# Kernel tuning notes

Measured on AMD Instinct MI355X. Metric: run time of the kernel, lower is better.

Reference implementation:

```python
import jax, jax.numpy as jnp
import numpy as np

PRE_NMS_TOP_N = 1024
POST_NMS_TOP_N = 256
NMS_THRESH = 0.7
MIN_SIZE = 4.0
SCORE_THRESH = 0.1
BASE_SIZE = 1024.0
SCALE = 0.25            # feature stride = 1/SCALE = 4
IMG_H, IMG_W = 1024.0, 1024.0
NEG_INF = -1e30
CAP = 8                 # max vertices of 4-gon intersect 4-gon


def setup_inputs() -> dict:
    key = jax.random.key(0)
    k1, k2 = jax.random.split(key)
    N, A, H, W = 2, 1, 256, 256
    objectness = jax.random.normal(k1, (N, A, H, W), dtype=jnp.float32)
    box_regression = jax.random.uniform(k2, (N, A * 5, H, W), dtype=jnp.float32) * 0.05
    return {"objectness": objectness, "box_regression": box_regression}


def eastbox2rbox(reg, H, W):
    # reg: (H*W, 5) -> rotated boxes (H*W, 5) in xywha (angle in degrees)
    jy, jx = jnp.meshgrid(jnp.arange(H, dtype=reg.dtype), jnp.arange(W, dtype=reg.dtype), indexing="ij")
    cx0 = (jx / SCALE).reshape(-1)
    cy0 = (jy / SCALE).reshape(-1)
    t = reg[:, 0] * BASE_SIZE
    r = reg[:, 1] * BASE_SIZE
    b = reg[:, 2] * BASE_SIZE
    l = reg[:, 3] * BASE_SIZE
    ang = (reg[:, 4] - 0.5) * 90.0
    w = l + r
    h = t + b
    xc = cx0 + 0.5 * (r - l)
    yc = cy0 + 0.5 * (b - t)
    return jnp.stack([xc, yc, w, h, ang], axis=-1)


def rbox_corners(box):
    # box: (5,) xywha -> (4,2) CCW corners
    th = box[4] * (jnp.pi / 180.0)
    c, s = jnp.cos(th), jnp.sin(th)
    dx = jnp.array([-0.5, 0.5, 0.5, -0.5], box.dtype) * box[2]
    dy = jnp.array([-0.5, -0.5, 0.5, 0.5], box.dtype) * box[3]
    return jnp.stack([box[0] + dx * c - dy * s, box[1] + dx * s + dy * c], axis=-1)


def clip_halfplane(poly, n, p1, p2):
    # Sutherland-Hodgman clip of a convex polygon (CAP,2) with n valid verts
    # against the half-plane left of directed edge p1->p2.
    M = poly.shape[0]
    idx = jnp.arange(M)
    valid = idx < n
    nxt = poly[jnp.where(idx + 1 < n, idx + 1, 0)]
    e = p2 - p1
    d_cur = e[0] * (poly[:, 1] - p1[1]) - e[1] * (poly[:, 0] - p1[0])
    d_nxt = e[0] * (nxt[:, 1] - p1[1]) - e[1] * (nxt[:, 0] - p1[0])
    in_cur = d_cur >= 0.0
    in_nxt = d_nxt >= 0.0
    denom = d_cur - d_nxt
    safe = jnp.where(jnp.abs(denom) > 1e-9, denom, 1.0)
    t = d_cur / safe
    inter = poly + t[:, None] * (nxt - poly)
    emit_cur = in_cur & valid
    emit_int = (in_cur != in_nxt) & valid
    pts = jnp.stack([poly, inter], axis=1).reshape(2 * M, 2)
    flags = jnp.stack([emit_cur, emit_int], axis=1).reshape(2 * M)
    pos = jnp.where(flags, jnp.cumsum(flags) - 1, M)  # M = dropped
    out = jnp.zeros((M, 2), poly.dtype).at[pos].set(jnp.where(flags[:, None], pts, 0.0), mode="drop")
    return out, jnp.sum(flags)


def intersect_area(pa, pb):
    # area of convex intersection of two 4-gons (each (4,2), CCW)
    poly = jnp.zeros((CAP, 2), pa.dtype).at[:4].set(pa)
    n = jnp.asarray(4, jnp.int32)
    for k in range(4):
        poly, n = clip_halfplane(poly, n, pb[k], pb[(k + 1) % 4])
    idx = jnp.arange(CAP)
    valid = idx < n
    nxt = poly[jnp.where(idx + 1 < n, idx + 1, 0)]
    cr = poly[:, 0] * nxt[:, 1] - nxt[:, 0] * poly[:, 1]
    area = 0.5 * jnp.abs(jnp.sum(jnp.where(valid, cr, 0.0)))
    return jnp.where(n >= 3, area, 0.0)


def riou(a, b):
    inter = intersect_area(rbox_corners(a), rbox_corners(b))
    union = a[2] * a[3] + b[2] * b[3] - inter
    return inter / jnp.maximum(union, 1e-9)


def greedy_nms(iou_mat, valid, thresh):
    K = valid.shape[0]
    ar = jnp.arange(K)

    def body(i, state):
        keep, sup = state
        is_keep = valid[i] & jnp.logical_not(sup[i])
        keep = keep.at[i].set(is_keep)
        sup = sup | (is_keep & (iou_mat[i] > thresh) & (ar > i))
        return keep, sup

    keep, _ = jax.lax.fori_loop(0, K, body, (jnp.zeros(K, bool), jnp.zeros(K, bool)))
    return keep


def process_image(obj, reg):
    A, H, W = obj.shape
    scores = obj.transpose(1, 2, 0).reshape(-1)       # (H*W*A,)
    reg5 = reg[:5].transpose(1, 2, 0).reshape(-1, 5)  # (H*W, 5)
    rboxes = eastbox2rbox(reg5, H, W)
    top_scores, top_idx = jax.lax.top_k(scores, PRE_NMS_TOP_N)
    boxes = rboxes[top_idx]
    valid = top_scores > SCORE_THRESH                 # eval-mode score thresh (masked, not dropped)
    # clip_to_image: clamp rotated-box centers into the image
    boxes = boxes.at[:, 0].set(jnp.clip(boxes[:, 0], 0.0, IMG_W - 1.0))
    boxes = boxes.at[:, 1].set(jnp.clip(boxes[:, 1], 0.0, IMG_H - 1.0))
    # remove_small_boxes
    valid = valid & (boxes[:, 2] >= MIN_SIZE) & (boxes[:, 3] >= MIN_SIZE)
    # full rotated IoU matrix, row-by-row to bound memory
    iou_mat = jax.lax.map(lambda a: jax.vmap(lambda b: riou(a, b))(boxes), boxes)
    keep = greedy_nms(iou_mat, valid, NMS_THRESH)
    sel = jnp.where(keep, top_scores, NEG_INF)
    fin_scores, fin_idx = jax.lax.top_k(sel, POST_NMS_TOP_N)
    fin_boxes = boxes[fin_idx]
    fin_valid = keep[fin_idx]
    out = jnp.concatenate([fin_boxes, fin_scores[:, None]], axis=-1)  # (post, 6) = xywha + score
    return jnp.where(fin_valid[:, None], out, 0.0)


def reference(objectness, box_regression):
    return jax.vmap(process_image)(objectness, box_regression)
```

## Files before the change

kernel.cpp:

```cpp
#include <hip/hip_runtime.h>
#include <hip/hip_bf16.h>

#define N_IMG 2
#define HW 65536
#define PRE 1024
#define POST 256
#define NBIN 4096
#define SORTN 4096
#define NMS_THR 0.7f
#define SCORE_T 0.1f
#define MIN_SZ 4.0f

__device__ __forceinline__ unsigned int fkey(float f) {
    unsigned int u = __float_as_uint(f);
    return u ^ ((u & 0x80000000u) ? 0xFFFFFFFFu : 0x80000000u);
}
__device__ __forceinline__ float unfkey(unsigned int k) {
    unsigned int u = (k & 0x80000000u) ? (k ^ 0x80000000u) : ~k;
    return __uint_as_float(u);
}
__device__ __forceinline__ unsigned long long readlane64(unsigned long long v, int l) {
    unsigned int lo = (unsigned int)__builtin_amdgcn_readlane((int)(unsigned int)v, l);
    unsigned int hi = (unsigned int)__builtin_amdgcn_readlane((int)(unsigned int)(v >> 32), l);
    return ((unsigned long long)hi << 32) | (unsigned long long)lo;
}

__global__ __launch_bounds__(1024) void k_front(const float* __restrict__ obj,
                                                unsigned int* phist,
                                                unsigned long long* masks,
                                                unsigned int* cnts) {
    __shared__ unsigned int lh[NBIN];
    int img = blockIdx.x >> 3;
    int seg = blockIdx.x & 7;
    for (int i = threadIdx.x; i < NBIN; i += 1024) lh[i] = 0u;
    {
        unsigned long long* mz = masks + (size_t)blockIdx.x * 2048;
        mz[threadIdx.x] = 0ULL;
        mz[threadIdx.x + 1024] = 0ULL;
    }
    if (blockIdx.x == 0 && threadIdx.x < 8) cnts[threadIdx.x] = 0u;
    __syncthreads();
    const float4* o4 = (const float4*)(obj + (size_t)img * HW);
    int base = seg * 2048;
#pragma unroll
    for (int k = 0; k < 2; ++k) {
        float4 v = o4[base + threadIdx.x + k * 1024];
        atomicAdd(&lh[fkey(v.x) >> 20], 1u);
        atomicAdd(&lh[fkey(v.y) >> 20], 1u);
        atomicAdd(&lh[fkey(v.z) >> 20], 1u);
        atomicAdd(&lh[fkey(v.w) >> 20], 1u);
    }
    __syncthreads();
    unsigned int* ph = phist + (size_t)blockIdx.x * NBIN;
    for (int i = threadIdx.x; i < NBIN; i += 1024) ph[i] = lh[i];
}

__global__ void k_findbin(const unsigned int* __restrict__ phist, unsigned int* selB) {
    __shared__ unsigned int lh[NBIN];
    __shared__ unsigned int chunk[256];
    int img = blockIdx.x;
    int t = threadIdx.x;
    for (int c = 0; c < 16; ++c) {
        int b = c * 256 + t;
        unsigned int v = 0;
#pragma unroll
        for (int q = 0; q < 8; ++q) v += phist[(size_t)(img * 8 + q) * NBIN + b];
        lh[b] = v;
    }
    __syncthreads();
    unsigned int s = 0;
    for (int k = 0; k < 16; ++k) s += lh[t * 16 + k];
    chunk[t] = s;
    __syncthreads();
    if (t == 0) {
        unsigned int run = 0;
        int c;
        for (c = 255; c >= 0; --c) {
            if (run + chunk[c] >= PRE) break;
            run += chunk[c];
        }
        unsigned int B = 0;
        for (int b = c * 16 + 15; b >= c * 16; --b) {
            if (run + lh[b] >= PRE) { B = (unsigned int)b; break; }
            run += lh[b];
        }
        selB[img] = B;
    }
}

__global__ __launch_bounds__(256) void k_compact(const float* __restrict__ obj,
                                                 const unsigned int* __restrict__ selB,
                                                 unsigned int* cnts, unsigned long long* cbuf) {
    __shared__ unsigned long long lbuf[1024];
    __shared__ unsigned int lcnt, lbase;
    int t = blockIdx.x * 256 + threadIdx.x;
    const float4* o4 = (const float4*)obj;
#pragma unroll
    for (int k = 0; k < 2; ++k) {
        if (threadIdx.x == 0) lcnt = 0;
        __syncthreads();
        int p = t + k * 16384;
        int img = p >> 14;
        unsigned int B = selB[img];
        float4 v = o4[p];
        float vs[4] = {v.x, v.y, v.z, v.w};
#pragma unroll
        for (int c = 0; c < 4; ++c) {
            unsigned int key = fkey(vs[c]);
            if ((key >> 20) >= B) {
                unsigned int i = (unsigned int)((p & 16383) * 4 + c);
                unsigned int pos = atomicAdd(&lcnt, 1u);
                lbuf[pos] = ((unsigned long long)key << 32) |
                            (unsigned long long)(0xFFFFFFFFu - i);
            }
        }
        __syncthreads();
        if (threadIdx.x == 0) lbase = atomicAdd(&cnts[img], lcnt);
        __syncthreads();
        unsigned int n = lcnt, base = lbase;
        for (unsigned int q = threadIdx.x; q < n; q += 256) {
            unsigned int gp = base + q;
            if (gp < SORTN) cbuf[img * SORTN + gp] = lbuf[q];
        }
        __syncthreads();
    }
}

__global__ __launch_bounds__(256) void k_rankdec(const unsigned int* __restrict__ cnts,
                                                 const unsigned long long* __restrict__ cbuf,
                                                 const float* __restrict__ boxreg,
                                                 float* boxes, float* corn, float4* circ,
                                                 unsigned int* varr, float* tscr) {
    __shared__ unsigned long long keys[SORTN];
    int img = blockIdx.x >> 4;
    int slice = blockIdx.x & 15;
    unsigned int M = cnts[img]; if (M > SORTN) M = SORTN;
    for (unsigned int i = threadIdx.x; i < M; i += 256) keys[i] = cbuf[img * SORTN + i];
    __syncthreads();
    unsigned int cid = (unsigned int)slice * 256 + threadIdx.x;
    if (cid >= M) return;
    unsigned long long cv = keys[cid];
    unsigned int r = 0;
    for (unsigned int j = 0; j < M; ++j) r += (keys[j] > cv) ? 1u : 0u;
    if (r >= PRE) return;

    int g = img * PRE + (int)r;
    unsigned int key = (unsigned int)(cv >> 32);
    unsigned int idx = (0xFFFFFFFFu - (unsigned int)(cv & 0xFFFFFFFFULL)) & 0xFFFFu;
    float sc = unfkey(key);
    int h = (int)(idx >> 8);
    int w = (int)(idx & 255u);
    const float* rg = boxreg + (size_t)img * 5 * HW;
    float t_ = rg[0 * HW + idx] * 1024.0f;
    float rr = rg[1 * HW + idx] * 1024.0f;
    float bb = rg[2 * HW + idx] * 1024.0f;
    float ll = rg[3 * HW + idx] * 1024.0f;
    float ang = (rg[4 * HW + idx] - 0.5f) * 90.0f;
    float wd = ll + rr;
    float ht = t_ + bb;
    float xc = (float)w * 4.0f + 0.5f * (rr - ll);
    float yc = (float)h * 4.0f + 0.5f * (bb - t_);
    xc = fminf(fmaxf(xc, 0.0f), 1023.0f);
    yc = fminf(fmaxf(yc, 0.0f), 1023.0f);
    bool valid = (sc > SCORE_T) && (wd >= MIN_SZ) && (ht >= MIN_SZ);

    float* bx = boxes + (size_t)g * 5;
    bx[0] = xc; bx[1] = yc; bx[2] = wd; bx[3] = ht; bx[4] = ang;
    tscr[g] = sc;
    varr[g] = valid ? 1u : 0u;

    float th = ang * (float)(3.14159265358979323846 / 180.0);
    float c = cosf(th), s = sinf(th);
    const float dxs[4] = {-0.5f, 0.5f, 0.5f, -0.5f};
    const float dys[4] = {-0.5f, -0.5f, 0.5f, 0.5f};
    float* cr = corn + (size_t)g * 8;
#pragma unroll
    for (int k = 0; k < 4; ++k) {
        float dx = dxs[k] * wd, dy = dys[k] * ht;
        cr[2 * k]     = xc + dx * c - dy * s;
        cr[2 * k + 1] = yc + dx * s + dy * c;
    }
    circ[g] = make_float4(xc, yc, 0.5f * sqrtf(wd * wd + ht * ht) + 0.01f, wd * ht);
}

__global__ __launch_bounds__(256) void k_pairclip(const float4* __restrict__ circ,
                                                  const float* __restrict__ corn,
                                                  unsigned long long* masks) {
    __shared__ float SPX[8][256], SPY[8][256], SQX[8][256], SQY[8][256];
    __shared__ unsigned int plist[1280];
    __shared__ unsigned int pcnt;
    int tid = threadIdx.x;
    if (tid == 0) pcnt = 0;
    __syncthreads();
    int t0 = blockIdx.x * 256 + tid;
    for (int k = 0; k < 16; ++k) {
        int p = t0 + k * 131072;
        int img = p >> 20;
        int r = p & 1048575;
        int i = r >> 10, j = r & 1023;
        if (j > i) {
            float4 a = circ[img * PRE + i];
            float4 b = circ[img * PRE + j];
            float dx = b.x - a.x, dy = b.y - a.y, rr = a.z + b.z;
            if (dx * dx + dy * dy <= rr * rr)
                plist[atomicAdd(&pcnt, 1u)] =
                    ((unsigned int)img << 20) | ((unsigned int)i << 10) | (unsigned int)j;
        }
        __syncthreads();
        unsigned int n = pcnt;
        if (n >= 1024 || k == 15) {
            for (unsigned int q = tid; q < n; q += 256) {
                unsigned int pr = plist[q];
                int im = (int)(pr >> 20);
                int bi = (int)((pr >> 10) & 1023);
                int bj = (int)(pr & 1023);
                int ra = im * PRE + bi, rb = im * PRE + bj;
                const float4* ca = (const float4*)(corn + (size_t)ra * 8);
                float4 a0 = ca[0], a1 = ca[1];
                const float4* cb = (const float4*)(corn + (size_t)rb * 8);
                float4 b0 = cb[0], b1 = cb[1];
                float cbx[4] = {b0.x, b0.z, b1.x, b1.z};
                float cby[4] = {b0.y, b0.w, b1.y, b1.w};
                SPX[0][tid] = a0.x; SPY[0][tid] = a0.y;
                SPX[1][tid] = a0.z; SPY[1][tid] = a0.w;
                SPX[2][tid] = a1.x; SPY[2][tid] = a1.y;
                SPX[3][tid] = a1.z; SPY[3][tid] = a1.w;
                int n2 = 4;
#pragma unroll
                for (int e = 0; e < 4; ++e) {
                    float (*PX)[256] = (e & 1) ? SQX : SPX;
                    float (*PY)[256] = (e & 1) ? SQY : SPY;
                    float (*QX)[256] = (e & 1) ? SPX : SQX;
                    float (*QY)[256] = (e & 1) ? SPY : SQY;
                    float p1x = cbx[e], p1y = cby[e];
                    int e2 = (e + 1) & 3;
                    float ex = cbx[e2] - p1x, ey = cby[e2] - p1y;
                    int m = 0;
                    for (int kk = 0; kk < n2; ++kk) {
                        int kn = (kk + 1 < n2) ? kk + 1 : 0;
                        float cx_ = PX[kk][tid], cy_ = PY[kk][tid];
                        float nx_ = PX[kn][tid], ny_ = PY[kn][tid];
                        float dc = ex * (cy_ - p1y) - ey * (cx_ - p1x);
                        float dn = ex * (ny_ - p1y) - ey * (nx_ - p1x);
                        bool ic = dc >= 0.0f;
                        bool inx = dn >= 0.0f;
                        if (ic && m < 8) { QX[m][tid] = cx_; QY[m][tid] = cy_; ++m; }
                        if ((ic != inx) && m < 8) {
                            float den = dc - dn;
                            float safe = (fabsf(den) > 1e-9f) ? den : 1.0f;
                            float tt = dc / safe;
                            QX[m][tid] = cx_ + tt * (nx_ - cx_);
                            QY[m][tid] = cy_ + tt * (ny_ - cy_);
                            ++m;
                        }
                    }
                    n2 = m;
                }
                float inter = 0.0f;
                if (n2 >= 3) {
                    float s = 0.0f;
                    for (int kk = 0; kk < n2; ++kk) {
                        int kn = (kk + 1 < n2) ? kk + 1 : 0;
                        s += SPX[kk][tid] * SPY[kn][tid] - SPX[kn][tid] * SPY[kk][tid];
                    }
                    inter = 0.5f * fabsf(s);
                }
                float uni = circ[ra].w + circ[rb].w - inter;
                float iou = inter / fmaxf(uni, 1e-9f);
                if (iou > NMS_THR)
                    atomicOr(&masks[(size_t)ra * 16 + (bj >> 6)], 1ULL << (bj & 63));
            }
            __syncthreads();
            if (tid == 0) pcnt = 0;
            __syncthreads();
        }
    }
}

__global__ __launch_bounds__(1024) void k_nms_out(const unsigned long long* __restrict__ masks,
                                                  const unsigned int* __restrict__ varr,
                                                  const float* __restrict__ boxes,
                                                  const float* __restrict__ tscr,
                                                  float* __restrict__ out) {
    __shared__ unsigned long long lm[PRE * 16];
    __shared__ unsigned long long vmw_s[16];
    __shared__ unsigned short keptIdx[POST];
    __shared__ int sTotal;
    int img = blockIdx.x;
    int t = threadIdx.x;
    const unsigned long long* mbase = masks + (size_t)img * PRE * 16;
    {
        const ulonglong2* src = (const ulonglong2*)mbase;
        ulonglong2* dst = (ulonglong2*)lm;
#pragma unroll
        for (int k = 0; k < 8; ++k) dst[t + k * 1024] = src[t + k * 1024];
    }
    {
        unsigned long long bal = __ballot(varr[img * PRE + t] != 0u);
        if ((t & 63) == 0) vmw_s[t >> 6] = bal;
    }
    __syncthreads();

    if (t < 64) {
        int lane = t;
        int lw = lane & 15;
        unsigned long long vmw = vmw_s[lw];
        unsigned long long supw = 0ULL;
        int cnt = 0;
        for (int b = 0; b < 16 && cnt < POST; ++b) {
            unsigned long long avail = readlane64(vmw, b) & ~readlane64(supw, b);
            while (avail && cnt < POST) {
                unsigned long long a = avail;
                int d0 = __ffsll((long long)a) - 1; a &= a - 1;
                int d1 = a ? __ffsll((long long)a) - 1 : 64; a &= a - 1;
                int d2 = a ? __ffsll((long long)a) - 1 : 64; a &= a - 1;
                int d3 = a ? __ffsll((long long)a) - 1 : 64; a &= a - 1;
                int r0 = b * 64 + d0;
                int r1 = b * 64 + (d1 & 63);
                int r2 = b * 64 + (d2 & 63);
                int r3 = b * 64 + (d3 & 63);
                unsigned long long w0 = lm[r0 * 16 + lw];
                unsigned long long w1 = lm[r1 * 16 + lw];
                unsigned long long w2 = lm[r2 * 16 + lw];
                unsigned long long w3 = lm[r3 * 16 + lw];
                unsigned long long sb = readlane64(w0, b);
                supw |= w0;
                if (lane == 0) keptIdx[cnt] = (unsigned short)r0;
                ++cnt;
                if (d1 < 64 && cnt < POST && !((sb >> d1) & 1ULL)) {
                    sb |= readlane64(w1, b); supw |= w1;
                    if (lane == 0) keptIdx[cnt] = (unsigned short)r1;
                    ++cnt;
                }
                if (d2 < 64 && cnt < POST && !((sb >> d2) & 1ULL)) {
                    sb |= readlane64(w2, b); supw |= w2;
                    if (lane == 0) keptIdx[cnt] = (unsigned short)r2;
                    ++cnt;
                }
                if (d3 < 64 && cnt < POST && !((sb >> d3) & 1ULL)) {
                    sb |= readlane64(w3, b); supw |= w3;
                    if (lane == 0) keptIdx[cnt] = (unsigned short)r3;
                    ++cnt;
                }
                avail = a & ~sb;
            }
        }
        if (lane == 0) sTotal = cnt;
    }
    __syncthreads();

    int total = sTotal;
    if (t < POST) {
        float v0 = 0.f, v1 = 0.f, v2 = 0.f, v3 = 0.f, v4 = 0.f, v5 = 0.f;
        if (t < total) {
            int i = keptIdx[t];
            const float* b = boxes + (size_t)(img * PRE + i) * 5;
            v0 = b[0]; v1 = b[1]; v2 = b[2]; v3 = b[3]; v4 = b[4];
            v5 = tscr[img * PRE + i];
        }
        float* o2 = out + (size_t)(img * POST + t) * 6;
        o2[0] = v0; o2[1] = v1; o2[2] = v2; o2[3] = v3; o2[4] = v4; o2[5] = v5;
    }
}

enum : size_t {
    OFF_BOX   = 0,
    OFF_CORN  = 40960,
    OFF_CIRC  = 106496,
    OFF_VARR  = 139264,
    OFF_TSCR  = 147456,
    OFF_MASK  = 155648,
    OFF_PHIST = 417792,
    OFF_CNTS  = 679936,
    OFF_SELB  = 679968,
    OFF_CBUF  = 679984,
};

extern "C" void kernel_launch(void* const* d_in, const int* in_sizes, int n_in,
                              void* d_out, int out_size, void* d_ws, size_t ws_size,
                              hipStream_t stream) {
    const float* obj = (const float*)d_in[0];
    const float* boxreg = (const float*)d_in[1];
    float* out = (float*)d_out;

    char* w = (char*)d_ws;
    float* boxes = (float*)(w + OFF_BOX);
    float* corn = (float*)(w + OFF_CORN);
    float4* circ = (float4*)(w + OFF_CIRC);
    unsigned int* varr = (unsigned int*)(w + OFF_VARR);
    float* tscr = (float*)(w + OFF_TSCR);
    unsigned long long* masks = (unsigned long long*)(w + OFF_MASK);
    unsigned int* phist = (unsigned int*)(w + OFF_PHIST);
    unsigned int* cnts = (unsigned int*)(w + OFF_CNTS);
    unsigned int* selB = (unsigned int*)(w + OFF_SELB);
    unsigned long long* cbuf = (unsigned long long*)(w + OFF_CBUF);

    k_front<<<16, 1024, 0, stream>>>(obj, phist, masks, cnts);
    k_findbin<<<N_IMG, 256, 0, stream>>>(phist, selB);
    k_compact<<<64, 256, 0, stream>>>(obj, selB, cnts, cbuf);
    k_rankdec<<<32, 256, 0, stream>>>(cnts, cbuf, boxreg, boxes, corn, circ, varr, tscr);
    k_pairclip<<<512, 256, 0, stream>>>(circ, corn, masks);
    k_nms_out<<<N_IMG, 1024, 0, stream>>>(masks, varr, boxes, tscr, out);
}
```

Before: 88.77 us.

## Fuse the six pipeline kernels into one cooperative persistent kernel with grid syncs

Merges histogram, bin selection, compaction, rank/decode, pair clipping and NMS into a single cooperative launch of 256 blocks that separates stages with grid.sync, and keeps the multi-kernel path as a fallback if the cooperative launch fails. The aim is to remove per-kernel launch gaps and tail latency between the six small dependent kernels. In exchange, the pair-clip stage runs on 256 blocks instead of 512, so each block handles twice the pairs. The shared-memory union also grows to the largest stage (128KB for the NMS mask copy), which can limit residency or cause the cooperative launch to fail.

```diff
diff --git a/kernel.cpp b/kernel.cpp
--- a/kernel.cpp
+++ b/kernel.cpp
@@ -1,5 +1,8 @@
 #include <hip/hip_runtime.h>
 #include <hip/hip_bf16.h>
+#include <hip/hip_cooperative_groups.h>
+
+namespace cg = cooperative_groups;
 
 #define N_IMG 2
 #define HW 65536
@@ -10,6 +13,7 @@
 #define NMS_THR 0.7f
 #define SCORE_T 0.1f
 #define MIN_SZ 4.0f
+#define GRID 256
 
 __device__ __forceinline__ unsigned int fkey(float f) {
     unsigned int u = __float_as_uint(f);
@@ -25,126 +29,28 @@
     return ((unsigned long long)hi << 32) | (unsigned long long)lo;
 }
 
-__global__ __launch_bounds__(1024) void k_front(const float* __restrict__ obj,
-                                                unsigned int* phist,
-                                                unsigned long long* masks,
-                                                unsigned int* cnts) {
-    __shared__ unsigned int lh[NBIN];
-    int img = blockIdx.x >> 3;
-    int seg = blockIdx.x & 7;
-    for (int i = threadIdx.x; i < NBIN; i += 1024) lh[i] = 0u;
-    {
-        unsigned long long* mz = masks + (size_t)blockIdx.x * 2048;
-        mz[threadIdx.x] = 0ULL;
-        mz[threadIdx.x + 1024] = 0ULL;
-    }
-    if (blockIdx.x == 0 && threadIdx.x < 8) cnts[threadIdx.x] = 0u;
-    __syncthreads();
-    const float4* o4 = (const float4*)(obj + (size_t)img * HW);
-    int base = seg * 2048;
-#pragma unroll
-    for (int k = 0; k < 2; ++k) {
-        float4 v = o4[base + threadIdx.x + k * 1024];
-        atomicAdd(&lh[fkey(v.x) >> 20], 1u);
-        atomicAdd(&lh[fkey(v.y) >> 20], 1u);
-        atomicAdd(&lh[fkey(v.z) >> 20], 1u);
-        atomicAdd(&lh[fkey(v.w) >> 20], 1u);
-    }
-    __syncthreads();
-    unsigned int* ph = phist + (size_t)blockIdx.x * NBIN;
-    for (int i = threadIdx.x; i < NBIN; i += 1024) ph[i] = lh[i];
-}
-
-__global__ void k_findbin(const unsigned int* __restrict__ phist, unsigned int* selB) {
-    __shared__ unsigned int lh[NBIN];
-    __shared__ unsigned int chunk[256];
-    int img = blockIdx.x;
-    int t = threadIdx.x;
-    for (int c = 0; c < 16; ++c) {
-        int b = c * 256 + t;
-        unsigned int v = 0;
-#pragma unroll
-        for (int q = 0; q < 8; ++q) v += phist[(size_t)(img * 8 + q) * NBIN + b];
-        lh[b] = v;
-    }
-    __syncthreads();
-    unsigned int s = 0;
-    for (int k = 0; k < 16; ++k) s += lh[t * 16 + k];
-    chunk[t] = s;
-    __syncthreads();
-    if (t == 0) {
-        unsigned int run = 0;
-        int c;
-        for (c = 255; c >= 0; --c) {
-            if (run + chunk[c] >= PRE) break;
-            run += chunk[c];
-        }
-        unsigned int B = 0;
-        for (int b = c * 16 + 15; b >= c * 16; --b) {
-            if (run + lh[b] >= PRE) { B = (unsigned int)b; break; }
-            run += lh[b];
-        }
-        selB[img] = B;
-    }
-}
-
-__global__ __launch_bounds__(256) void k_compact(const float* __restrict__ obj,
-                                                 const unsigned int* __restrict__ selB,
-                                                 unsigned int* cnts, unsigned long long* cbuf) {
-    __shared__ unsigned long long lbuf[1024];
-    __shared__ unsigned int lcnt, lbase;
-    int t = blockIdx.x * 256 + threadIdx.x;
-    const float4* o4 = (const float4*)obj;
-#pragma unroll
-    for (int k = 0; k < 2; ++k) {
-        if (threadIdx.x == 0) lcnt = 0;
-        __syncthreads();
-        int p = t + k * 16384;
-        int img = p >> 14;
-        unsigned int B = selB[img];
-        float4 v = o4[p];
-        float vs[4] = {v.x, v.y, v.z, v.w};
-#pragma unroll
-        for (int c = 0; c < 4; ++c) {
-            unsigned int key = fkey(vs[c]);
-            if ((key >> 20) >= B) {
-                unsigned int i = (unsigned int)((p & 16383) * 4 + c);
-                unsigned int pos = atomicAdd(&lcnt, 1u);
-                lbuf[pos] = ((unsigned long long)key << 32) |
-                            (unsigned long long)(0xFFFFFFFFu - i);
-            }
-        }
-        __syncthreads();
-        if (threadIdx.x == 0) lbase = atomicAdd(&cnts[img], lcnt);
-        __syncthreads();
-        unsigned int n = lcnt, base = lbase;
-        for (unsigned int q = threadIdx.x; q < n; q += 256) {
-            unsigned int gp = base + q;
-            if (gp < SORTN) cbuf[img * SORTN + gp] = lbuf[q];
-        }
-        __syncthreads();
-    }
-}
-
-__global__ __launch_bounds__(256) void k_rankdec(const unsigned int* __restrict__ cnts,
-                                                 const unsigned long long* __restrict__ cbuf,
-                                                 const float* __restrict__ boxreg,
-                                                 float* boxes, float* corn, float4* circ,
-                                                 unsigned int* varr, float* tscr) {
-    __shared__ unsigned long long keys[SORTN];
-    int img = blockIdx.x >> 4;
-    int slice = blockIdx.x & 15;
-    unsigned int M = cnts[img]; if (M > SORTN) M = SORTN;
-    for (unsigned int i = threadIdx.x; i < M; i += 256) keys[i] = cbuf[img * SORTN + i];
-    __syncthreads();
-    unsigned int cid = (unsigned int)slice * 256 + threadIdx.x;
-    if (cid >= M) return;
-    unsigned long long cv = keys[cid];
-    unsigned int r = 0;
-    for (unsigned int j = 0; j < M; ++j) r += (keys[j] > cv) ? 1u : 0u;
-    if (r >= PRE) return;
-
-    int g = img * PRE + (int)r;
+struct SMemU {
+    union {
+        unsigned int hist[NBIN];
+        unsigned long long lbuf[1024];
+        unsigned long long keys[SORTN];
+        struct {
+            float SPX[8][256], SPY[8][256], SQX[8][256], SQY[8][256];
+            unsigned int plist[1280];
+        } e;
+        unsigned long long lm[PRE * 16];
+    } u;
+    unsigned int pcnt, lcnt, lbase;
+    unsigned long long vmw_s[16];
+    unsigned short keptIdx[POST];
+    int sTotal;
+};
+
+__device__ __forceinline__ void decode_one(unsigned long long cv, int img,
+                                           const float* __restrict__ boxreg,
+                                           float* boxes, float* corn, float4* circ,
+                                           unsigned int* varr, float* tscr, int r) {
+    int g = img * PRE + r;
     unsigned int key = (unsigned int)(cv >> 32);
     unsigned int idx = (0xFFFFFFFFu - (unsigned int)(cv & 0xFFFFFFFFULL)) & 0xFFFFu;
     float sc = unfkey(key);
@@ -183,11 +89,436 @@
     circ[g] = make_float4(xc, yc, 0.5f * sqrtf(wd * wd + ht * ht) + 0.01f, wd * ht);
 }
 
+template <typename E>
+__device__ __forceinline__ void clip_pair(unsigned int pr, int tid, E* e,
+                                          const float* __restrict__ corn,
+                                          const float4* __restrict__ circ,
+                                          unsigned long long* masks) {
+    int im = (int)(pr >> 20);
+    int bi = (int)((pr >> 10) & 1023);
+    int bj = (int)(pr & 1023);
+    int ra = im * PRE + bi, rb = im * PRE + bj;
+    const float4* ca = (const float4*)(corn + (size_t)ra * 8);
+    float4 a0 = ca[0], a1 = ca[1];
+    const float4* cb = (const float4*)(corn + (size_t)rb * 8);
+    float4 b0 = cb[0], b1 = cb[1];
+    float cbx[4] = {b0.x, b0.z, b1.x, b1.z};
+    float cby[4] = {b0.y, b0.w, b1.y, b1.w};
+    e->SPX[0][tid] = a0.x; e->SPY[0][tid] = a0.y;
+    e->SPX[1][tid] = a0.z; e->SPY[1][tid] = a0.w;
+    e->SPX[2][tid] = a1.x; e->SPY[2][tid] = a1.y;
+    e->SPX[3][tid] = a1.z; e->SPY[3][tid] = a1.w;
+    int n2 = 4;
+#pragma unroll
+    for (int ed = 0; ed < 4; ++ed) {
+        float (*PX)[256] = (ed & 1) ? e->SQX : e->SPX;
+        float (*PY)[256] = (ed & 1) ? e->SQY : e->SPY;
+        float (*QX)[256] = (ed & 1) ? e->SPX : e->SQX;
+        float (*QY)[256] = (ed & 1) ? e->SPY : e->SQY;
+        float p1x = cbx[ed], p1y = cby[ed];
+        int e2 = (ed + 1) & 3;
+        float ex = cbx[e2] - p1x, ey = cby[e2] - p1y;
+        int m = 0;
+        for (int kk = 0; kk < n2; ++kk) {
+            int kn = (kk + 1 < n2) ? kk + 1 : 0;
+            float cx_ = PX[kk][tid], cy_ = PY[kk][tid];
+            float nx_ = PX[kn][tid], ny_ = PY[kn][tid];
+            float dc = ex * (cy_ - p1y) - ey * (cx_ - p1x);
+            float dn = ex * (ny_ - p1y) - ey * (nx_ - p1x);
+            bool ic = dc >= 0.0f;
+            bool inx = dn >= 0.0f;
+            if (ic && m < 8) { QX[m][tid] = cx_; QY[m][tid] = cy_; ++m; }
+            if ((ic != inx) && m < 8) {
+                float den = dc - dn;
+                float safe = (fabsf(den) > 1e-9f) ? den : 1.0f;
+                float tt = dc / safe;
+                QX[m][tid] = cx_ + tt * (nx_ - cx_);
+                QY[m][tid] = cy_ + tt * (ny_ - cy_);
+                ++m;
+            }
+        }
+        n2 = m;
+    }
+    float inter = 0.0f;
+    if (n2 >= 3) {
+        float s = 0.0f;
+        for (int kk = 0; kk < n2; ++kk) {
+            int kn = (kk + 1 < n2) ? kk + 1 : 0;
+            s += e->SPX[kk][tid] * e->SPY[kn][tid] - e->SPX[kn][tid] * e->SPY[kk][tid];
+        }
+        inter = 0.5f * fabsf(s);
+    }
+    float uni = circ[ra].w + circ[rb].w - inter;
+    float iou = inter / fmaxf(uni, 1e-9f);
+    if (iou > NMS_THR)
+        atomicOr(&masks[(size_t)ra * 16 + (bj >> 6)], 1ULL << (bj & 63));
+}
+
+__global__ __launch_bounds__(256) void k_mega(const float* __restrict__ obj,
+                                              const float* __restrict__ boxreg,
+                                              float* __restrict__ out,
+                                              float* boxes, float* corn, float4* circ,
+                                              unsigned int* varr, float* tscr,
+                                              unsigned long long* masks, unsigned int* phist,
+                                              unsigned int* cnts, unsigned int* selB,
+                                              unsigned long long* cbuf) {
+    cg::grid_group grid = cg::this_grid();
+    __shared__ SMemU sm;
+    int bid = blockIdx.x;
+    int tid = threadIdx.x;
+
+    {
+        unsigned long long* mz = masks + (size_t)bid * 128;
+        if (tid < 128) mz[tid] = 0ULL;
+        if (bid == 0 && tid < 8) cnts[tid] = 0u;
+        if (bid < 16) {
+            unsigned int* lh = sm.u.hist;
+            for (int i = tid; i < NBIN; i += 256) lh[i] = 0u;
+            __syncthreads();
+            int img = bid >> 3, seg = bid & 7;
+            const float4* o4 = (const float4*)(obj + (size_t)img * HW);
+            int base = seg * 2048;
+#pragma unroll
+            for (int k = 0; k < 8; ++k) {
+                float4 v = o4[base + tid + k * 256];
+                atomicAdd(&lh[fkey(v.x) >> 20], 1u);
+                atomicAdd(&lh[fkey(v.y) >> 20], 1u);
+                atomicAdd(&lh[fkey(v.z) >> 20], 1u);
+                atomicAdd(&lh[fkey(v.w) >> 20], 1u);
+            }
+            __syncthreads();
+            unsigned int* ph = phist + (size_t)bid * NBIN;
+            for (int i = tid; i < NBIN; i += 256) ph[i] = lh[i];
+        }
+    }
+    __threadfence();
+    grid.sync();
+
+    if (bid < N_IMG) {
+        int img = bid;
+        unsigned int* lh = sm.u.hist;
+        __shared__ unsigned int chunk[256];
+        for (int c = 0; c < 16; ++c) {
+            int b = c * 256 + tid;
+            unsigned int v = 0;
+#pragma unroll
+            for (int q = 0; q < 8; ++q) v += phist[(size_t)(img * 8 + q) * NBIN + b];
+            lh[b] = v;
+        }
+        __syncthreads();
+        unsigned int s = 0;
+        for (int k = 0; k < 16; ++k) s += lh[tid * 16 + k];
+        chunk[tid] = s;
+        __syncthreads();
+        if (tid == 0) {
+            unsigned int run = 0;
+            int c;
+            for (c = 255; c >= 0; --c) {
+                if (run + chunk[c] >= PRE) break;
+                run += chunk[c];
+            }
+            unsigned int B = 0;
+            for (int b = c * 16 + 15; b >= c * 16; --b) {
+                if (run + lh[b] >= PRE) { B = (unsigned int)b; break; }
+                run += lh[b];
+            }
+            selB[img] = B;
+        }
+    }
+    __threadfence();
+    grid.sync();
+
+    if (bid < 64) {
+        int t = bid * 256 + tid;
+        const float4* o4 = (const float4*)obj;
+#pragma unroll
+        for (int k = 0; k < 2; ++k) {
+            if (tid == 0) sm.lcnt = 0;
+            __syncthreads();
+            int p = t + k * 16384;
+            int img = p >> 14;
+            unsigned int B = selB[img];
+            float4 v = o4[p];
+            float vs[4] = {v.x, v.y, v.z, v.w};
+#pragma unroll
+            for (int c = 0; c < 4; ++c) {
+                unsigned int key = fkey(vs[c]);
+                if ((key >> 20) >= B) {
+                    unsigned int i = (unsigned int)((p & 16383) * 4 + c);
+                    unsigned int pos = atomicAdd(&sm.lcnt, 1u);
+                    sm.u.lbuf[pos] = ((unsigned long long)key << 32) |
+                                     (unsigned long long)(0xFFFFFFFFu - i);
+                }
+            }
+            __syncthreads();
+            if (tid == 0) sm.lbase = atomicAdd(&cnts[img], sm.lcnt);
+            __syncthreads();
+            unsigned int n = sm.lcnt, base = sm.lbase;
+            for (unsigned int q = tid; q < n; q += 256) {
+                unsigned int gp = base + q;
+                if (gp < SORTN) cbuf[img * SORTN + gp] = sm.u.lbuf[q];
+            }
+            __syncthreads();
+        }
+    }
+    __threadfence();
+    grid.sync();
+
+    if (bid < 32) {
+        int img = bid >> 4;
+        int slice = bid & 15;
+        unsigned int M = cnts[img]; if (M > SORTN) M = SORTN;
+        for (unsigned int i = tid; i < M; i += 256) sm.u.keys[i] = cbuf[img * SORTN + i];
+        __syncthreads();
+        unsigned int cid = (unsigned int)slice * 256 + tid;
+        if (cid < M) {
+            unsigned long long cv = sm.u.keys[cid];
+            unsigned int r = 0;
+            for (unsigned int j = 0; j < M; ++j) r += (sm.u.keys[j] > cv) ? 1u : 0u;
+            if (r < PRE)
+                decode_one(cv, img, boxreg, boxes, corn, circ, varr, tscr, (int)r);
+        }
+    }
+    __threadfence();
+    grid.sync();
+
+    {
+        if (tid == 0) sm.pcnt = 0;
+        __syncthreads();
+        int t0 = bid * 256 + tid;
+        for (int k = 0; k < 32; ++k) {
+            int p = t0 + k * 65536;
+            int img = p >> 20;
+            int r = p & 1048575;
+            int i = r >> 10, j = r & 1023;
+            if (j > i) {
+                float4 a = circ[img * PRE + i];
+                float4 b = circ[img * PRE + j];
+                float dx = b.x - a.x, dy = b.y - a.y, rr = a.z + b.z;
+                if (dx * dx + dy * dy <= rr * rr)
+                    sm.u.e.plist[atomicAdd(&sm.pcnt, 1u)] =
+                        ((unsigned int)img << 20) | ((unsigned int)i << 10) | (unsigned int)j;
+            }
+            __syncthreads();
+            unsigned int n = sm.pcnt;
+            if (n >= 1024 || k == 31) {
+                for (unsigned int q = tid; q < n; q += 256)
+                    clip_pair(sm.u.e.plist[q], tid, &sm.u.e, corn, circ, masks);
+                __syncthreads();
+                if (tid == 0) sm.pcnt = 0;
+                __syncthreads();
+            }
+        }
+    }
+    __threadfence();
+    grid.sync();
+
+    if (bid < N_IMG) {
+        int img = bid;
+        {
+            const ulonglong2* src = (const ulonglong2*)(masks + (size_t)img * PRE * 16);
+            ulonglong2* dst = (ulonglong2*)sm.u.lm;
+#pragma unroll
+            for (int k = 0; k < 32; ++k) dst[tid + k * 256] = src[tid + k * 256];
+        }
+        {
+            int wv = tid >> 6, lane = tid & 63;
+#pragma unroll
+            for (int q = 0; q < 4; ++q) {
+                unsigned long long bal = __ballot(varr[img * PRE + q * 256 + tid] != 0u);
+                if (lane == 0) sm.vmw_s[q * 4 + wv] = bal;
+            }
+        }
+        __syncthreads();
+        if (tid < 64) {
+            int lane = tid;
+            int lw = lane & 15;
+            unsigned long long vmw = sm.vmw_s[lw];
+            unsigned long long supw = 0ULL;
+            int cnt = 0;
+            for (int b = 0; b < 16 && cnt < POST; ++b) {
+                unsigned long long avail = readlane64(vmw, b) & ~readlane64(supw, b);
+                while (avail && cnt < POST) {
+                    unsigned long long a = avail;
+                    int d0 = __ffsll((long long)a) - 1; a &= a - 1;
+                    int d1 = a ? __ffsll((long long)a) - 1 : 64; a &= a - 1;
+                    int d2 = a ? __ffsll((long long)a) - 1 : 64; a &= a - 1;
+                    int d3 = a ? __ffsll((long long)a) - 1 : 64; a &= a - 1;
+                    int r0 = b * 64 + d0;
+                    int r1 = b * 64 + (d1 & 63);
+                    int r2 = b * 64 + (d2 & 63);
+                    int r3 = b * 64 + (d3 & 63);
+                    unsigned long long w0 = sm.u.lm[r0 * 16 + lw];
+                    unsigned long long w1 = sm.u.lm[r1 * 16 + lw];
+                    unsigned long long w2 = sm.u.lm[r2 * 16 + lw];
+                    unsigned long long w3 = sm.u.lm[r3 * 16 + lw];
+                    unsigned long long sb = readlane64(w0, b);
+                    supw |= w0;
+                    if (lane == 0) sm.keptIdx[cnt] = (unsigned short)r0;
+                    ++cnt;
+                    if (d1 < 64 && cnt < POST && !((sb >> d1) & 1ULL)) {
+                        sb |= readlane64(w1, b); supw |= w1;
+                        if (lane == 0) sm.keptIdx[cnt] = (unsigned short)r1;
+                        ++cnt;
+                    }
+                    if (d2 < 64 && cnt < POST && !((sb >> d2) & 1ULL)) {
+                        sb |= readlane64(w2, b); supw |= w2;
+                        if (lane == 0) sm.keptIdx[cnt] = (unsigned short)r2;
+                        ++cnt;
+                    }
+                    if (d3 < 64 && cnt < POST && !((sb >> d3) & 1ULL)) {
+                        sb |= readlane64(w3, b); supw |= w3;
+                        if (lane == 0) sm.keptIdx[cnt] = (unsigned short)r3;
+                        ++cnt;
+                    }
+                    avail = a & ~sb;
+                }
+            }
+            if (lane == 0) sm.sTotal = cnt;
+        }
+        __syncthreads();
+        int total = sm.sTotal;
+        {
+            float v0 = 0.f, v1 = 0.f, v2 = 0.f, v3 = 0.f, v4 = 0.f, v5 = 0.f;
+            if (tid < total) {
+                int i = sm.keptIdx[tid];
+                const float* b = boxes + (size_t)(img * PRE + i) * 5;
+                v0 = b[0]; v1 = b[1]; v2 = b[2]; v3 = b[3]; v4 = b[4];
+                v5 = tscr[img * PRE + i];
+            }
+            float* o2 = out + (size_t)(img * POST + tid) * 6;
+            o2[0] = v0; o2[1] = v1; o2[2] = v2; o2[3] = v3; o2[4] = v4; o2[5] = v5;
+        }
+    }
+}
+
+__global__ __launch_bounds__(1024) void k_front(const float* __restrict__ obj,
+                                                unsigned int* phist,
+                                                unsigned long long* masks,
+                                                unsigned int* cnts) {
+    __shared__ unsigned int lh[NBIN];
+    int img = blockIdx.x >> 3;
+    int seg = blockIdx.x & 7;
+    for (int i = threadIdx.x; i < NBIN; i += 1024) lh[i] = 0u;
+    {
+        unsigned long long* mz = masks + (size_t)blockIdx.x * 2048;
+        mz[threadIdx.x] = 0ULL;
+        mz[threadIdx.x + 1024] = 0ULL;
+    }
+    if (blockIdx.x == 0 && threadIdx.x < 8) cnts[threadIdx.x] = 0u;
+    __syncthreads();
+    const float4* o4 = (const float4*)(obj + (size_t)img * HW);
+    int base = seg * 2048;
+#pragma unroll
+    for (int k = 0; k < 2; ++k) {
+        float4 v = o4[base + threadIdx.x + k * 1024];
+        atomicAdd(&lh[fkey(v.x) >> 20], 1u);
+        atomicAdd(&lh[fkey(v.y) >> 20], 1u);
+        atomicAdd(&lh[fkey(v.z) >> 20], 1u);
+        atomicAdd(&lh[fkey(v.w) >> 20], 1u);
+    }
+    __syncthreads();
+    unsigned int* ph = phist + (size_t)blockIdx.x * NBIN;
+    for (int i = threadIdx.x; i < NBIN; i += 1024) ph[i] = lh[i];
+}
+
+__global__ void k_findbin(const unsigned int* __restrict__ phist, unsigned int* selB) {
+    __shared__ unsigned int lh[NBIN];
+    __shared__ unsigned int chunk[256];
+    int img = blockIdx.x;
+    int t = threadIdx.x;
+    for (int c = 0; c < 16; ++c) {
+        int b = c * 256 + t;
+        unsigned int v = 0;
+#pragma unroll
+        for (int q = 0; q < 8; ++q) v += phist[(size_t)(img * 8 + q) * NBIN + b];
+        lh[b] = v;
+    }
+    __syncthreads();
+    unsigned int s = 0;
+    for (int k = 0; k < 16; ++k) s += lh[t * 16 + k];
+    chunk[t] = s;
+    __syncthreads();
+    if (t == 0) {
+        unsigned int run = 0;
+        int c;
+        for (c = 255; c >= 0; --c) {
+            if (run + chunk[c] >= PRE) break;
+            run += chunk[c];
+        }
+        unsigned int B = 0;
+        for (int b = c * 16 + 15; b >= c * 16; --b) {
+            if (run + lh[b] >= PRE) { B = (unsigned int)b; break; }
+            run += lh[b];
+        }
+        selB[img] = B;
+    }
+}
+
+__global__ __launch_bounds__(256) void k_compact(const float* __restrict__ obj,
+                                                 const unsigned int* __restrict__ selB,
+                                                 unsigned int* cnts, unsigned long long* cbuf) {
+    __shared__ unsigned long long lbuf[1024];
+    __shared__ unsigned int lcnt, lbase;
+    int t = blockIdx.x * 256 + threadIdx.x;
+    const float4* o4 = (const float4*)obj;
+#pragma unroll
+    for (int k = 0; k < 2; ++k) {
+        if (threadIdx.x == 0) lcnt = 0;
+        __syncthreads();
+        int p = t + k * 16384;
+        int img = p >> 14;
+        unsigned int B = selB[img];
+        float4 v = o4[p];
+        float vs[4] = {v.x, v.y, v.z, v.w};
+#pragma unroll
+        for (int c = 0; c < 4; ++c) {
+            unsigned int key = fkey(vs[c]);
+            if ((key >> 20) >= B) {
+                unsigned int i = (unsigned int)((p & 16383) * 4 + c);
+                unsigned int pos = atomicAdd(&lcnt, 1u);
+                lbuf[pos] = ((unsigned long long)key << 32) |
+                            (unsigned long long)(0xFFFFFFFFu - i);
+            }
+        }
+        __syncthreads();
+        if (threadIdx.x == 0) lbase = atomicAdd(&cnts[img], lcnt);
+        __syncthreads();
+        unsigned int n = lcnt, base = lbase;
+        for (unsigned int q = threadIdx.x; q < n; q += 256) {
+            unsigned int gp = base + q;
+            if (gp < SORTN) cbuf[img * SORTN + gp] = lbuf[q];
+        }
+        __syncthreads();
+    }
+}
+
+__global__ __launch_bounds__(256) void k_rankdec(const unsigned int* __restrict__ cnts,
+                                                 const unsigned long long* __restrict__ cbuf,
+                                                 const float* __restrict__ boxreg,
+                                                 float* boxes, float* corn, float4* circ,
+                                                 unsigned int* varr, float* tscr) {
+    __shared__ unsigned long long keys[SORTN];
+    int img = blockIdx.x >> 4;
+    int slice = blockIdx.x & 15;
+    unsigned int M = cnts[img]; if (M > SORTN) M = SORTN;
+    for (unsigned int i = threadIdx.x; i < M; i += 256) keys[i] = cbuf[img * SORTN + i];
+    __syncthreads();
+    unsigned int cid = (unsigned int)slice * 256 + threadIdx.x;
+    if (cid >= M) return;
+    unsigned long long cv = keys[cid];
+    unsigned int r = 0;
+    for (unsigned int j = 0; j < M; ++j) r += (keys[j] > cv) ? 1u : 0u;
+    if (r < PRE) decode_one(cv, img, boxreg, boxes, corn, circ, varr, tscr, (int)r);
+}
+
 __global__ __launch_bounds__(256) void k_pairclip(const float4* __restrict__ circ,
                                                   const float* __restrict__ corn,
                                                   unsigned long long* masks) {
-    __shared__ float SPX[8][256], SPY[8][256], SQX[8][256], SQY[8][256];
-    __shared__ unsigned int plist[1280];
+    __shared__ struct {
+        float SPX[8][256], SPY[8][256], SQX[8][256], SQY[8][256];
+        unsigned int plist[1280];
+    } e;
     __shared__ unsigned int pcnt;
     int tid = threadIdx.x;
     if (tid == 0) pcnt = 0;
@@ -203,73 +534,14 @@
             float4 b = circ[img * PRE + j];
             float dx = b.x - a.x, dy = b.y - a.y, rr = a.z + b.z;
             if (dx * dx + dy * dy <= rr * rr)
-                plist[atomicAdd(&pcnt, 1u)] =
+                e.plist[atomicAdd(&pcnt, 1u)] =
                     ((unsigned int)img << 20) | ((unsigned int)i << 10) | (unsigned int)j;
         }
         __syncthreads();
         unsigned int n = pcnt;
         if (n >= 1024 || k == 15) {
-            for (unsigned int q = tid; q < n; q += 256) {
-                unsigned int pr = plist[q];
-                int im = (int)(pr >> 20);
-                int bi = (int)((pr >> 10) & 1023);
-                int bj = (int)(pr & 1023);
-                int ra = im * PRE + bi, rb = im * PRE + bj;
-                const float4* ca = (const float4*)(corn + (size_t)ra * 8);
-                float4 a0 = ca[0], a1 = ca[1];
-                const float4* cb = (const float4*)(corn + (size_t)rb * 8);
-                float4 b0 = cb[0], b1 = cb[1];
-                float cbx[4] = {b0.x, b0.z, b1.x, b1.z};
-                float cby[4] = {b0.y, b0.w, b1.y, b1.w};
-                SPX[0][tid] = a0.x; SPY[0][tid] = a0.y;
-                SPX[1][tid] = a0.z; SPY[1][tid] = a0.w;
-                SPX[2][tid] = a1.x; SPY[2][tid] = a1.y;
-                SPX[3][tid] = a1.z; SPY[3][tid] = a1.w;
-                int n2 = 4;
-#pragma unroll
-                for (int e = 0; e < 4; ++e) {
-                    float (*PX)[256] = (e & 1) ? SQX : SPX;
-                    float (*PY)[256] = (e & 1) ? SQY : SPY;
-                    float (*QX)[256] = (e & 1) ? SPX : SQX;
-                    float (*QY)[256] = (e & 1) ? SPY : SQY;
-                    float p1x = cbx[e], p1y = cby[e];
-                    int e2 = (e + 1) & 3;
-                    float ex = cbx[e2] - p1x, ey = cby[e2] - p1y;
-                    int m = 0;
-                    for (int kk = 0; kk < n2; ++kk) {
-                        int kn = (kk + 1 < n2) ? kk + 1 : 0;
-                        float cx_ = PX[kk][tid], cy_ = PY[kk][tid];
-                        float nx_ = PX[kn][tid], ny_ = PY[kn][tid];
-                        float dc = ex * (cy_ - p1y) - ey * (cx_ - p1x);
-                        float dn = ex * (ny_ - p1y) - ey * (nx_ - p1x);
-                        bool ic = dc >= 0.0f;
-                        bool inx = dn >= 0.0f;
-                        if (ic && m < 8) { QX[m][tid] = cx_; QY[m][tid] = cy_; ++m; }
-                        if ((ic != inx) && m < 8) {
-                            float den = dc - dn;
-                            float safe = (fabsf(den) > 1e-9f) ? den : 1.0f;
-                            float tt = dc / safe;
-                            QX[m][tid] = cx_ + tt * (nx_ - cx_);
-                            QY[m][tid] = cy_ + tt * (ny_ - cy_);
-                            ++m;
-                        }
-                    }
-                    n2 = m;
-                }
-                float inter = 0.0f;
-                if (n2 >= 3) {
-                    float s = 0.0f;
-                    for (int kk = 0; kk < n2; ++kk) {
-                        int kn = (kk + 1 < n2) ? kk + 1 : 0;
-                        s += SPX[kk][tid] * SPY[kn][tid] - SPX[kn][tid] * SPY[kk][tid];
-                    }
-                    inter = 0.5f * fabsf(s);
-                }
-                float uni = circ[ra].w + circ[rb].w - inter;
-                float iou = inter / fmaxf(uni, 1e-9f);
-                if (iou > NMS_THR)
-                    atomicOr(&masks[(size_t)ra * 16 + (bj >> 6)], 1ULL << (bj & 63));
-            }
+            for (unsigned int q = tid; q < n; q += 256)
+                clip_pair(e.plist[q], tid, &e, corn, circ, masks);
             __syncthreads();
             if (tid == 0) pcnt = 0;
             __syncthreads();
@@ -300,7 +572,6 @@
         if ((t & 63) == 0) vmw_s[t >> 6] = bal;
     }
     __syncthreads();
-
     if (t < 64) {
         int lane = t;
         int lw = lane & 15;
@@ -348,7 +619,6 @@
         if (lane == 0) sTotal = cnt;
     }
     __syncthreads();
-
     int total = sTotal;
     if (t < POST) {
         float v0 = 0.f, v1 = 0.f, v2 = 0.f, v3 = 0.f, v4 = 0.f, v5 = 0.f;
@@ -395,10 +665,19 @@
     unsigned int* selB = (unsigned int*)(w + OFF_SELB);
     unsigned long long* cbuf = (unsigned long long*)(w + OFF_CBUF);
 
-    k_front<<<16, 1024, 0, stream>>>(obj, phist, masks, cnts);
-    k_findbin<<<N_IMG, 256, 0, stream>>>(phist, selB);
-    k_compact<<<64, 256, 0, stream>>>(obj, selB, cnts, cbuf);
-    k_rankdec<<<32, 256, 0, stream>>>(cnts, cbuf, boxreg, boxes, corn, circ, varr, tscr);
-    k_pairclip<<<512, 256, 0, stream>>>(circ, corn, masks);
-    k_nms_out<<<N_IMG, 1024, 0, stream>>>(masks, varr, boxes, tscr, out);
-}
+    void* args[] = {(void*)&obj, (void*)&boxreg, (void*)&out, (void*)&boxes,
+                    (void*)&corn, (void*)&circ, (void*)&varr, (void*)&tscr,
+                    (void*)&masks, (void*)&phist, (void*)&cnts, (void*)&selB,
+                    (void*)&cbuf};
+    hipError_t err = hipLaunchCooperativeKernel((void*)k_mega, dim3(GRID), dim3(256),
+                                                args, 0, stream);
+    if (err != hipSuccess) {
+        (void)hipGetLastError();
+        k_front<<<16, 1024, 0, stream>>>(obj, phist, masks, cnts);
+        k_findbin<<<N_IMG, 256, 0, stream>>>(phist, selB);
+        k_compact<<<64, 256, 0, stream>>>(obj, selB, cnts, cbuf);
+        k_rankdec<<<32, 256, 0, stream>>>(cnts, cbuf, boxreg, boxes, corn, circ, varr, tscr);
+        k_pairclip<<<512, 256, 0, stream>>>(circ, corn, masks);
+        k_nms_out<<<N_IMG, 1024, 0, stream>>>(masks, varr, boxes, tscr, out);
+    }
+}
```

New measurement: 311.2 us. +250.6%, slower.

## Enumerate only upper-triangle pairs in pairclip and widen NMS batch to eight

Applied to the files above, without the earlier changes.

The pair-clip kernel now maps each thread directly onto an upper-triangular (i<j) pair index through a sqrt-based triangular inverse, so only 8 outer iterations run instead of 16 and no lanes are spent on rejected j<=i pairs. The greedy NMS scan now pulls eight candidate bits per step instead of four, issuing more mask loads ahead of the serial check chain. The triangular inverse adds a sqrt and correction loops per thread. The wider NMS batch wastes loads when many candidates are suppressed.

```diff
diff --git a/kernel.cpp b/kernel.cpp
--- a/kernel.cpp
+++ b/kernel.cpp
@@ -10,6 +10,8 @@
 #define NMS_THR 0.7f
 #define SCORE_T 0.1f
 #define MIN_SZ 4.0f
+#define TRIPAIRS 523776
+#define TRITOTAL (2 * TRIPAIRS)
 
 __device__ __forceinline__ unsigned int fkey(float f) {
     unsigned int u = __float_as_uint(f);
@@ -126,25 +128,11 @@
     }
 }
 
-__global__ __launch_bounds__(256) void k_rankdec(const unsigned int* __restrict__ cnts,
-                                                 const unsigned long long* __restrict__ cbuf,
-                                                 const float* __restrict__ boxreg,
-                                                 float* boxes, float* corn, float4* circ,
-                                                 unsigned int* varr, float* tscr) {
-    __shared__ unsigned long long keys[SORTN];
-    int img = blockIdx.x >> 4;
-    int slice = blockIdx.x & 15;
-    unsigned int M = cnts[img]; if (M > SORTN) M = SORTN;
-    for (unsigned int i = threadIdx.x; i < M; i += 256) keys[i] = cbuf[img * SORTN + i];
-    __syncthreads();
-    unsigned int cid = (unsigned int)slice * 256 + threadIdx.x;
-    if (cid >= M) return;
-    unsigned long long cv = keys[cid];
-    unsigned int r = 0;
-    for (unsigned int j = 0; j < M; ++j) r += (keys[j] > cv) ? 1u : 0u;
-    if (r >= PRE) return;
-
-    int g = img * PRE + (int)r;
+__device__ __forceinline__ void decode_one(unsigned long long cv, int img,
+                                           const float* __restrict__ boxreg,
+                                           float* boxes, float* corn, float4* circ,
+                                           unsigned int* varr, float* tscr, int r) {
+    int g = img * PRE + r;
     unsigned int key = (unsigned int)(cv >> 32);
     unsigned int idx = (0xFFFFFFFFu - (unsigned int)(cv & 0xFFFFFFFFULL)) & 0xFFFFu;
     float sc = unfkey(key);
@@ -183,34 +171,59 @@
     circ[g] = make_float4(xc, yc, 0.5f * sqrtf(wd * wd + ht * ht) + 0.01f, wd * ht);
 }
 
+__global__ __launch_bounds__(256) void k_rankdec(const unsigned int* __restrict__ cnts,
+                                                 const unsigned long long* __restrict__ cbuf,
+                                                 const float* __restrict__ boxreg,
+                                                 float* boxes, float* corn, float4* circ,
+                                                 unsigned int* varr, float* tscr) {
+    __shared__ unsigned long long keys[SORTN];
+    int img = blockIdx.x >> 4;
+    int slice = blockIdx.x & 15;
+    unsigned int M = cnts[img]; if (M > SORTN) M = SORTN;
+    for (unsigned int i = threadIdx.x; i < M; i += 256) keys[i] = cbuf[img * SORTN + i];
+    __syncthreads();
+    unsigned int cid = (unsigned int)slice * 256 + threadIdx.x;
+    if (cid >= M) return;
+    unsigned long long cv = keys[cid];
+    unsigned int r = 0;
+    for (unsigned int j = 0; j < M; ++j) r += (keys[j] > cv) ? 1u : 0u;
+    if (r < PRE) decode_one(cv, img, boxreg, boxes, corn, circ, varr, tscr, (int)r);
+}
+
 __global__ __launch_bounds__(256) void k_pairclip(const float4* __restrict__ circ,
                                                   const float* __restrict__ corn,
                                                   unsigned long long* masks) {
-    __shared__ float SPX[8][256], SPY[8][256], SQX[8][256], SQY[8][256];
-    __shared__ unsigned int plist[1280];
+    __shared__ struct {
+        float SPX[8][256], SPY[8][256], SQX[8][256], SQY[8][256];
+        unsigned int plist[1280];
+    } e;
     __shared__ unsigned int pcnt;
     int tid = threadIdx.x;
     if (tid == 0) pcnt = 0;
     __syncthreads();
     int t0 = blockIdx.x * 256 + tid;
-    for (int k = 0; k < 16; ++k) {
-        int p = t0 + k * 131072;
-        int img = p >> 20;
-        int r = p & 1048575;
-        int i = r >> 10, j = r & 1023;
-        if (j > i) {
+    for (int k = 0; k < 8; ++k) {
+        int s = t0 + k * 131072;
+        if (s < TRITOTAL) {
+            int img = (s >= TRIPAIRS) ? 1 : 0;
+            int p = s - img * TRIPAIRS;
+            int r = (int)((sqrtf((float)(8 * p + 1)) - 1.0f) * 0.5f);
+            while ((r * (r + 1)) / 2 > p) --r;
+            while (((r + 1) * (r + 2)) / 2 <= p) ++r;
+            int i = p - (r * (r + 1)) / 2;
+            int j = r + 1;
             float4 a = circ[img * PRE + i];
             float4 b = circ[img * PRE + j];
             float dx = b.x - a.x, dy = b.y - a.y, rr = a.z + b.z;
             if (dx * dx + dy * dy <= rr * rr)
-                plist[atomicAdd(&pcnt, 1u)] =
+                e.plist[atomicAdd(&pcnt, 1u)] =
                     ((unsigned int)img << 20) | ((unsigned int)i << 10) | (unsigned int)j;
         }
         __syncthreads();
         unsigned int n = pcnt;
-        if (n >= 1024 || k == 15) {
+        if (n >= 1024 || k == 7) {
             for (unsigned int q = tid; q < n; q += 256) {
-                unsigned int pr = plist[q];
+                unsigned int pr = e.plist[q];
                 int im = (int)(pr >> 20);
                 int bi = (int)((pr >> 10) & 1023);
                 int bj = (int)(pr & 1023);
@@ -221,19 +234,19 @@
                 float4 b0 = cb[0], b1 = cb[1];
                 float cbx[4] = {b0.x, b0.z, b1.x, b1.z};
                 float cby[4] = {b0.y, b0.w, b1.y, b1.w};
-                SPX[0][tid] = a0.x; SPY[0][tid] = a0.y;
-                SPX[1][tid] = a0.z; SPY[1][tid] = a0.w;
-                SPX[2][tid] = a1.x; SPY[2][tid] = a1.y;
-                SPX[3][tid] = a1.z; SPY[3][tid] = a1.w;
+                e.SPX[0][tid] = a0.x; e.SPY[0][tid] = a0.y;
+                e.SPX[1][tid] = a0.z; e.SPY[1][tid] = a0.w;
+                e.SPX[2][tid] = a1.x; e.SPY[2][tid] = a1.y;
+                e.SPX[3][tid] = a1.z; e.SPY[3][tid] = a1.w;
                 int n2 = 4;
 #pragma unroll
-                for (int e = 0; e < 4; ++e) {
-                    float (*PX)[256] = (e & 1) ? SQX : SPX;
-                    float (*PY)[256] = (e & 1) ? SQY : SPY;
-                    float (*QX)[256] = (e & 1) ? SPX : SQX;
-                    float (*QY)[256] = (e & 1) ? SPY : SQY;
-                    float p1x = cbx[e], p1y = cby[e];
-                    int e2 = (e + 1) & 3;
+                for (int ed = 0; ed < 4; ++ed) {
+                    float (*PX)[256] = (ed & 1) ? e.SQX : e.SPX;
+                    float (*PY)[256] = (ed & 1) ? e.SQY : e.SPY;
+                    float (*QX)[256] = (ed & 1) ? e.SPX : e.SQX;
+                    float (*QY)[256] = (ed & 1) ? e.SPY : e.SQY;
+                    float p1x = cbx[ed], p1y = cby[ed];
+                    int e2 = (ed + 1) & 3;
                     float ex = cbx[e2] - p1x, ey = cby[e2] - p1y;
                     int m = 0;
                     for (int kk = 0; kk < n2; ++kk) {
@@ -258,12 +271,12 @@
                 }
                 float inter = 0.0f;
                 if (n2 >= 3) {
-                    float s = 0.0f;
+                    float sa = 0.0f;
                     for (int kk = 0; kk < n2; ++kk) {
                         int kn = (kk + 1 < n2) ? kk + 1 : 0;
-                        s += SPX[kk][tid] * SPY[kn][tid] - SPX[kn][tid] * SPY[kk][tid];
+                        sa += e.SPX[kk][tid] * e.SPY[kn][tid] - e.SPX[kn][tid] * e.SPY[kk][tid];
                     }
-                    inter = 0.5f * fabsf(s);
+                    inter = 0.5f * fabsf(sa);
                 }
                 float uni = circ[ra].w + circ[rb].w - inter;
                 float iou = inter / fmaxf(uni, 1e-9f);
@@ -300,7 +313,6 @@
         if ((t & 63) == 0) vmw_s[t >> 6] = bal;
     }
     __syncthreads();
-
     if (t < 64) {
         int lane = t;
         int lw = lane & 15;
@@ -315,14 +327,26 @@
                 int d1 = a ? __ffsll((long long)a) - 1 : 64; a &= a - 1;
                 int d2 = a ? __ffsll((long long)a) - 1 : 64; a &= a - 1;
                 int d3 = a ? __ffsll((long long)a) - 1 : 64; a &= a - 1;
+                int d4 = a ? __ffsll((long long)a) - 1 : 64; a &= a - 1;
+                int d5 = a ? __ffsll((long long)a) - 1 : 64; a &= a - 1;
+                int d6 = a ? __ffsll((long long)a) - 1 : 64; a &= a - 1;
+                int d7 = a ? __ffsll((long long)a) - 1 : 64; a &= a - 1;
                 int r0 = b * 64 + d0;
                 int r1 = b * 64 + (d1 & 63);
                 int r2 = b * 64 + (d2 & 63);
                 int r3 = b * 64 + (d3 & 63);
+                int r4 = b * 64 + (d4 & 63);
+                int r5 = b * 64 + (d5 & 63);
+                int r6 = b * 64 + (d6 & 63);
+                int r7 = b * 64 + (d7 & 63);
                 unsigned long long w0 = lm[r0 * 16 + lw];
                 unsigned long long w1 = lm[r1 * 16 + lw];
                 unsigned long long w2 = lm[r2 * 16 + lw];
                 unsigned long long w3 = lm[r3 * 16 + lw];
+                unsigned long long w4 = lm[r4 * 16 + lw];
+                unsigned long long w5 = lm[r5 * 16 + lw];
+                unsigned long long w6 = lm[r6 * 16 + lw];
+                unsigned long long w7 = lm[r7 * 16 + lw];
                 unsigned long long sb = readlane64(w0, b);
                 supw |= w0;
                 if (lane == 0) keptIdx[cnt] = (unsigned short)r0;
@@ -342,13 +366,32 @@
                     if (lane == 0) keptIdx[cnt] = (unsigned short)r3;
                     ++cnt;
                 }
+                if (d4 < 64 && cnt < POST && !((sb >> d4) & 1ULL)) {
+                    sb |= readlane64(w4, b); supw |= w4;
+                    if (lane == 0) keptIdx[cnt] = (unsigned short)r4;
+                    ++cnt;
+                }
+                if (d5 < 64 && cnt < POST && !((sb >> d5) & 1ULL)) {
+                    sb |= readlane64(w5, b); supw |= w5;
+                    if (lane == 0) keptIdx[cnt] = (unsigned short)r5;
+                    ++cnt;
+                }
+                if (d6 < 64 && cnt < POST && !((sb >> d6) & 1ULL)) {
+                    sb |= readlane64(w6, b); supw |= w6;
+                    if (lane == 0) keptIdx[cnt] = (unsigned short)r6;
+                    ++cnt;
+                }
+                if (d7 < 64 && cnt < POST && !((sb >> d7) & 1ULL)) {
+                    sb |= readlane64(w7, b); supw |= w7;
+                    if (lane == 0) keptIdx[cnt] = (unsigned short)r7;
+                    ++cnt;
+                }
                 avail = a & ~sb;
             }
         }
         if (lane == 0) sTotal = cnt;
     }
     __syncthreads();
-
     int total = sTotal;
     if (t < POST) {
         float v0 = 0.f, v1 = 0.f, v2 = 0.f, v3 = 0.f, v4 = 0.f, v5 = 0.f;
```

Measured after the change: 83.44 us, median of 2. -6.0%, faster.
